# Performance work log

Hardware: AMD Instinct MI355X
Metric: run time of the kernel (lower is better)

Reference implementation:

```python
import jax, jax.numpy as jnp
import numpy as np

G = 128            # grid_size (hardcoded in NeRFRenderer.__init__)
T = 32             # time_size (reduced from 64 to keep working set < 4GB)
CAS = 1            # cascade = 1 + ceil(log2(bound)), bound = 1
DECAY = 0.95
DENSITY_SCALE = 1.0
DENSITY_THRESH = 0.01


def _expand_bits(v):
    # instant-ngp style 10-bit -> 30-bit expansion (works for 7-bit coords of G=128)
    v = (v * jnp.uint32(0x00010001)) & jnp.uint32(0xFF0000FF)
    v = (v * jnp.uint32(0x00000101)) & jnp.uint32(0x0F00F00F)
    v = (v * jnp.uint32(0x00000011)) & jnp.uint32(0xC30C30C3)
    v = (v * jnp.uint32(0x00000005)) & jnp.uint32(0x49249249)
    return v


def _morton3d(coords):
    # coords: [N, 3] int32 in [0, G)
    x = _expand_bits(coords[:, 0].astype(jnp.uint32))
    y = _expand_bits(coords[:, 1].astype(jnp.uint32))
    z = _expand_bits(coords[:, 2].astype(jnp.uint32))
    return (x | (y << 1) | (z << 2)).astype(jnp.int32)


def setup_inputs() -> dict:
    key = jax.random.key(0)
    k1, k2 = jax.random.split(key)
    density_grid = jax.random.normal(k1, (T, CAS, G ** 3), dtype=jnp.float32) * 0.5
    sigmas = jax.random.uniform(k2, (T, CAS, G ** 3), dtype=jnp.float32)
    return {"density_grid": density_grid, "sigmas": sigmas}


def reference(density_grid, sigmas):
    # full-grid branch of update_extra_state (iter_density < 16)
    g = jnp.arange(G, dtype=jnp.int32)
    xx, yy, zz = jnp.meshgrid(g, g, g, indexing='ij')
    coords = jnp.stack([xx.ravel(), yy.ravel(), zz.ravel()], axis=-1)  # [G^3, 3]
    indices = _morton3d(coords)                                        # [G^3]

    # tmp_grid = -1; tmp_grid[t, cas, indices] = sigmas * density_scale
    tmp_grid = -jnp.ones_like(density_grid)
    tmp_grid = tmp_grid.at[:, :, indices].set(sigmas * DENSITY_SCALE)

    # decay / max merge on mutually-valid cells
    valid = (density_grid >= 0) & (tmp_grid >= 0)
    new_grid = jnp.where(valid, jnp.maximum(density_grid * DECAY, tmp_grid), density_grid)

    # threshold + packbits into bitfield (8 cells per byte, morton order)
    mean_density = jnp.mean(jnp.clip(new_grid, 0.0))
    thresh = jnp.minimum(mean_density, jnp.float32(DENSITY_THRESH))
    bits = (new_grid > thresh).reshape(T, -1, 8)                       # [T, CAS*G^3/8, 8]
    weights = (jnp.int32(1) << jnp.arange(8, dtype=jnp.int32))
    bitfield = jnp.sum(bits.astype(jnp.int32) * weights, axis=-1)      # [T, CAS*G^3/8]
    return new_grid, bitfield
```

## Files before the change

### kernel.cpp

```cpp
#include <hip/hip_runtime.h>

#define G    128
#define G3   (G * G * G)
#define TDIM 32
#define NTOT (TDIM * G3)
#define NBYTES_OUT (NTOT / 8)
#define DECAY 0.95f
#define DTH   0.01f
#define NBLK1 (TDIM * 512)

__device__ __forceinline__ unsigned expand3(unsigned v) {
    v = (v * 0x00010001u) & 0xFF0000FFu;
    v = (v * 0x00000101u) & 0x0F00F00Fu;
    v = (v * 0x00000011u) & 0xC30C30C3u;
    v = (v * 0x00000005u) & 0x49249249u;
    return v;
}

__device__ __forceinline__ unsigned compact3(unsigned v) {
    v &= 0x49249249u;
    v = (v | (v >> 2))  & 0xC30C30C3u;
    v = (v | (v >> 4))  & 0x0F00F00Fu;
    v = (v | (v >> 8))  & 0xFF0000FFu;
    v = (v | (v >> 16)) & 0x000003FFu;
    return v;
}

__global__ __launch_bounds__(256) void
pass1(const float* __restrict__ dg, const float* __restrict__ sg,
      float* __restrict__ out_grid, float* __restrict__ out_bits,
      float* __restrict__ partials)
{
    __shared__ float smem[4096];
    const int blk  = blockIdx.x;
    const int t    = blk >> 9;
    const int cube = blk & 511;
    const int base = t * G3;

    const unsigned Xc = compact3((unsigned)cube);
    const unsigned Yc = compact3((unsigned)cube >> 1);
    const unsigned Zc = compact3((unsigned)cube >> 2);
    const int origin  = (int)((Xc << 18) | (Yc << 11) | (Zc << 4));
    const float* __restrict__ sgt = sg + base + origin;

    #pragma unroll
    for (int k = 0; k < 4; ++k) {
        const int c  = threadIdx.x + (k << 8);
        const int lx = c >> 6;
        const int ly = (c >> 2) & 15;
        const int lz = (c & 3) << 2;
        const float4 s = *reinterpret_cast<const float4*>(sgt + (lx << 14) + (ly << 7) + lz);
        const int m = (int)(expand3((unsigned)lx) | (expand3((unsigned)ly) << 1)
                          | (expand3((unsigned)lz) << 2));
        const int x = (((m >> 7) & 1) << 2) ^ (((m >> 8) & 1) << 3) ^ (((m >> 10) & 1) << 4);
        smem[m ^ x]        = s.x;
        smem[(m | 4) ^ x]  = s.y;
        smem[(m | 32) ^ x] = s.z;
        smem[(m | 36) ^ x] = s.w;
    }
    __syncthreads();

    float lsum = 0.f;
    #pragma unroll
    for (int k = 0; k < 4; ++k) {
        const int j  = (threadIdx.x + (k << 8)) << 2;
        const int xb = (((j >> 7) & 1) << 2) ^ (((j >> 8) & 1) << 3) ^ (((j >> 10) & 1) << 4);
        const float4 s = *reinterpret_cast<const float4*>(&smem[j ^ xb]);

        const int jg = base + (cube << 12) + j;
        const float4 v = *reinterpret_cast<const float4*>(dg + jg);

        float4 r;
        r.x = (v.x >= 0.f && s.x >= 0.f) ? fmaxf(v.x * DECAY, s.x) : v.x;
        r.y = (v.y >= 0.f && s.y >= 0.f) ? fmaxf(v.y * DECAY, s.y) : v.y;
        r.z = (v.z >= 0.f && s.z >= 0.f) ? fmaxf(v.z * DECAY, s.z) : v.z;
        r.w = (v.w >= 0.f && s.w >= 0.f) ? fmaxf(v.w * DECAY, s.w) : v.w;

        *reinterpret_cast<float4*>(out_grid + jg) = r;

        lsum += fmaxf(r.x, 0.f) + fmaxf(r.y, 0.f) + fmaxf(r.z, 0.f) + fmaxf(r.w, 0.f);

        int nib = (r.x > DTH ? 1 : 0) | (r.y > DTH ? 2 : 0) |
                  (r.z > DTH ? 4 : 0) | (r.w > DTH ? 8 : 0);
        int partner = __shfl_xor(nib, 1, 64);
        if ((threadIdx.x & 1) == 0)
            out_bits[jg >> 3] = (float)(nib | (partner << 4));
    }

    #pragma unroll
    for (int off = 32; off; off >>= 1) lsum += __shfl_down(lsum, off, 64);
    __shared__ float wsum[4];
    if ((threadIdx.x & 63) == 0) wsum[threadIdx.x >> 6] = lsum;
    __syncthreads();
    if (threadIdx.x == 0)
        partials[blk] = wsum[0] + wsum[1] + wsum[2] + wsum[3];
}

__global__ __launch_bounds__(1024) void
reduce_thresh(const float* __restrict__ partials, float* __restrict__ thresh)
{
    float s = 0.f;
    for (int i = threadIdx.x; i < NBLK1; i += 1024) s += partials[i];
    #pragma unroll
    for (int off = 32; off; off >>= 1) s += __shfl_down(s, off, 64);
    __shared__ float wsum[16];
    if ((threadIdx.x & 63) == 0) wsum[threadIdx.x >> 6] = s;
    __syncthreads();
    if (threadIdx.x == 0) {
        float tot = 0.f;
        #pragma unroll
        for (int i = 0; i < 16; ++i) tot += wsum[i];
        thresh[0] = fminf(tot / (float)NTOT, DTH);
    }
}

__global__ __launch_bounds__(256) void
fix_bits(const float* __restrict__ grid, const float* __restrict__ thresh,
         float* __restrict__ out_bits)
{
    const float th = thresh[0];
    if (th == DTH) return;
    const int n = blockIdx.x * 256 + threadIdx.x;
    const float4* g = reinterpret_cast<const float4*>(grid) + (n << 1);
    const float4 a = g[0], b = g[1];
    int byte = (a.x > th ? 1 : 0)   | (a.y > th ? 2 : 0)   |
               (a.z > th ? 4 : 0)   | (a.w > th ? 8 : 0)   |
               (b.x > th ? 16 : 0)  | (b.y > th ? 32 : 0)  |
               (b.z > th ? 64 : 0)  | (b.w > th ? 128 : 0);
    out_bits[n] = (float)byte;
}

extern "C" void kernel_launch(void* const* d_in, const int* in_sizes, int n_in,
                              void* d_out, int out_size, void* d_ws, size_t ws_size,
                              hipStream_t stream)
{
    const float* dg = (const float*)d_in[0];
    const float* sg = (const float*)d_in[1];
    float* out_grid = (float*)d_out;
    float* out_bits = out_grid + NTOT;
    float* partials = (float*)d_ws;
    float* thresh   = partials + NBLK1;

    pass1<<<NBLK1, 256, 0, stream>>>(dg, sg, out_grid, out_bits, partials);
    reduce_thresh<<<1, 1024, 0, stream>>>(partials, thresh);
    fix_bits<<<NBYTES_OUT / 256, 256, 0, stream>>>(out_grid, thresh, out_bits);
}
```

Before: 178.3 us.

## Issue density loads before the smem transpose, give each thread 16 contiguous cells, use nontemporal I/O

Each thread now owns 16 contiguous cells instead of four strided float4s. Its density_grid loads are issued at kernel start, before the sigma gather and barrier, so their latency overlaps the shared-memory transpose. Loads and stores use nontemporal builtins, and each thread writes two bitfield bytes directly, with no cross-lane shuffle. The launch bounds now request 6 waves per EU, and holding 16 values per thread raises register pressure. The per-thread contiguous access also changes the coalescing pattern of global memory traffic.

New measurement: 261.3 us. +46.5%, slower.

```diff
diff --git a/kernel.cpp b/kernel.cpp
--- a/kernel.cpp
+++ b/kernel.cpp
@@ -9,6 +9,9 @@
 #define DTH   0.01f
 #define NBLK1 (TDIM * 512)
 
+typedef float f32x4 __attribute__((ext_vector_type(4)));
+typedef float f32x2 __attribute__((ext_vector_type(2)));
+
 __device__ __forceinline__ unsigned expand3(unsigned v) {
     v = (v * 0x00010001u) & 0xFF0000FFu;
     v = (v * 0x00000101u) & 0x0F00F00Fu;
@@ -16,7 +19,6 @@
     v = (v * 0x00000005u) & 0x49249249u;
     return v;
 }
-
 __device__ __forceinline__ unsigned compact3(unsigned v) {
     v &= 0x49249249u;
     v = (v | (v >> 2))  & 0xC30C30C3u;
@@ -25,74 +27,99 @@
     v = (v | (v >> 16)) & 0x000003FFu;
     return v;
 }
+__device__ __forceinline__ int swz(int m) {
+    return (((m >> 7) & 1) << 2) ^ (((m >> 8) & 1) << 3) ^ (((m >> 10) & 1) << 4);
+}
 
-__global__ __launch_bounds__(256) void
+__device__ __forceinline__ f32x4 merge4(f32x4 v, f32x4 s) {
+    f32x4 r;
+    r.x = (v.x >= 0.f && s.x >= 0.f) ? fmaxf(v.x * DECAY, s.x) : v.x;
+    r.y = (v.y >= 0.f && s.y >= 0.f) ? fmaxf(v.y * DECAY, s.y) : v.y;
+    r.z = (v.z >= 0.f && s.z >= 0.f) ? fmaxf(v.z * DECAY, s.z) : v.z;
+    r.w = (v.w >= 0.f && s.w >= 0.f) ? fmaxf(v.w * DECAY, s.w) : v.w;
+    return r;
+}
+
+__global__ __launch_bounds__(256, 6) void
 pass1(const float* __restrict__ dg, const float* __restrict__ sg,
       float* __restrict__ out_grid, float* __restrict__ out_bits,
       float* __restrict__ partials)
 {
     __shared__ float smem[4096];
+    __shared__ float wsum[4];
     const int blk  = blockIdx.x;
     const int t    = blk >> 9;
     const int cube = blk & 511;
     const int base = t * G3;
+    const int tid  = threadIdx.x;
+    const int jg0  = base + (cube << 12) + (tid << 4);
+
+    const f32x4* dgp = reinterpret_cast<const f32x4*>(dg + jg0);
+    const f32x4 v0 = __builtin_nontemporal_load(dgp + 0);
+    const f32x4 v1 = __builtin_nontemporal_load(dgp + 1);
+    const f32x4 v2 = __builtin_nontemporal_load(dgp + 2);
+    const f32x4 v3 = __builtin_nontemporal_load(dgp + 3);
 
     const unsigned Xc = compact3((unsigned)cube);
     const unsigned Yc = compact3((unsigned)cube >> 1);
     const unsigned Zc = compact3((unsigned)cube >> 2);
-    const int origin  = (int)((Xc << 18) | (Yc << 11) | (Zc << 4));
-    const float* __restrict__ sgt = sg + base + origin;
-
+    const float* __restrict__ sgt = sg + base + (int)((Xc << 18) | (Yc << 11) | (Zc << 4));
     #pragma unroll
     for (int k = 0; k < 4; ++k) {
-        const int c  = threadIdx.x + (k << 8);
+        const int c  = tid + (k << 8);
         const int lx = c >> 6;
         const int ly = (c >> 2) & 15;
         const int lz = (c & 3) << 2;
-        const float4 s = *reinterpret_cast<const float4*>(sgt + (lx << 14) + (ly << 7) + lz);
-        const int m = (int)(expand3((unsigned)lx) | (expand3((unsigned)ly) << 1)
-                          | (expand3((unsigned)lz) << 2));
-        const int x = (((m >> 7) & 1) << 2) ^ (((m >> 8) & 1) << 3) ^ (((m >> 10) & 1) << 4);
-        smem[m ^ x]        = s.x;
-        smem[(m | 4) ^ x]  = s.y;
-        smem[(m | 32) ^ x] = s.z;
-        smem[(m | 36) ^ x] = s.w;
+        const f32x4 s = *reinterpret_cast<const f32x4*>(sgt + (lx << 14) + (ly << 7) + lz);
+        const int m  = (int)(expand3((unsigned)lx) | (expand3((unsigned)ly) << 1)
+                           | (expand3((unsigned)lz) << 2));
+        const int mb = m ^ swz(m);
+        smem[mb]      = s.x;
+        smem[mb ^ 4]  = s.y;
+        smem[mb ^ 32] = s.z;
+        smem[mb ^ 36] = s.w;
     }
     __syncthreads();
 
-    float lsum = 0.f;
-    #pragma unroll
-    for (int k = 0; k < 4; ++k) {
-        const int j  = (threadIdx.x + (k << 8)) << 2;
-        const int xb = (((j >> 7) & 1) << 2) ^ (((j >> 8) & 1) << 3) ^ (((j >> 10) & 1) << 4);
-        const float4 s = *reinterpret_cast<const float4*>(&smem[j ^ xb]);
+    const int j = tid << 4;
+    const int b = j ^ swz(j);
+    const f32x4 s0 = *reinterpret_cast<const f32x4*>(&smem[b]);
+    const f32x4 s1 = *reinterpret_cast<const f32x4*>(&smem[b ^ 4]);
+    const f32x4 s2 = *reinterpret_cast<const f32x4*>(&smem[b ^ 8]);
+    const f32x4 s3 = *reinterpret_cast<const f32x4*>(&smem[b ^ 12]);
 
-        const int jg = base + (cube << 12) + j;
-        const float4 v = *reinterpret_cast<const float4*>(dg + jg);
+    const f32x4 r0 = merge4(v0, s0);
+    const f32x4 r1 = merge4(v1, s1);
+    const f32x4 r2 = merge4(v2, s2);
+    const f32x4 r3 = merge4(v3, s3);
 
-        float4 r;
-        r.x = (v.x >= 0.f && s.x >= 0.f) ? fmaxf(v.x * DECAY, s.x) : v.x;
-        r.y = (v.y >= 0.f && s.y >= 0.f) ? fmaxf(v.y * DECAY, s.y) : v.y;
-        r.z = (v.z >= 0.f && s.z >= 0.f) ? fmaxf(v.z * DECAY, s.z) : v.z;
-        r.w = (v.w >= 0.f && s.w >= 0.f) ? fmaxf(v.w * DECAY, s.w) : v.w;
+    f32x4* ogp = reinterpret_cast<f32x4*>(out_grid + jg0);
+    __builtin_nontemporal_store(r0, ogp + 0);
+    __builtin_nontemporal_store(r1, ogp + 1);
+    __builtin_nontemporal_store(r2, ogp + 2);
+    __builtin_nontemporal_store(r3, ogp + 3);
 
-        *reinterpret_cast<float4*>(out_grid + jg) = r;
+    float lsum = fmaxf(r0.x, 0.f) + fmaxf(r0.y, 0.f) + fmaxf(r0.z, 0.f) + fmaxf(r0.w, 0.f)
+               + fmaxf(r1.x, 0.f) + fmaxf(r1.y, 0.f) + fmaxf(r1.z, 0.f) + fmaxf(r1.w, 0.f)
+               + fmaxf(r2.x, 0.f) + fmaxf(r2.y, 0.f) + fmaxf(r2.z, 0.f) + fmaxf(r2.w, 0.f)
+               + fmaxf(r3.x, 0.f) + fmaxf(r3.y, 0.f) + fmaxf(r3.z, 0.f) + fmaxf(r3.w, 0.f);
 
-        lsum += fmaxf(r.x, 0.f) + fmaxf(r.y, 0.f) + fmaxf(r.z, 0.f) + fmaxf(r.w, 0.f);
-
-        int nib = (r.x > DTH ? 1 : 0) | (r.y > DTH ? 2 : 0) |
-                  (r.z > DTH ? 4 : 0) | (r.w > DTH ? 8 : 0);
-        int partner = __shfl_xor(nib, 1, 64);
-        if ((threadIdx.x & 1) == 0)
-            out_bits[jg >> 3] = (float)(nib | (partner << 4));
-    }
+    const int byte0 = (r0.x > DTH ? 1 : 0)  | (r0.y > DTH ? 2 : 0)  |
+                      (r0.z > DTH ? 4 : 0)  | (r0.w > DTH ? 8 : 0)  |
+                      (r1.x > DTH ? 16 : 0) | (r1.y > DTH ? 32 : 0) |
+                      (r1.z > DTH ? 64 : 0) | (r1.w > DTH ? 128 : 0);
+    const int byte1 = (r2.x > DTH ? 1 : 0)  | (r2.y > DTH ? 2 : 0)  |
+                      (r2.z > DTH ? 4 : 0)  | (r2.w > DTH ? 8 : 0)  |
+                      (r3.x > DTH ? 16 : 0) | (r3.y > DTH ? 32 : 0) |
+                      (r3.z > DTH ? 64 : 0) | (r3.w > DTH ? 128 : 0);
+    f32x2 bb; bb.x = (float)byte0; bb.y = (float)byte1;
+    __builtin_nontemporal_store(bb, reinterpret_cast<f32x2*>(out_bits + (jg0 >> 3)));
 
     #pragma unroll
     for (int off = 32; off; off >>= 1) lsum += __shfl_down(lsum, off, 64);
-    __shared__ float wsum[4];
-    if ((threadIdx.x & 63) == 0) wsum[threadIdx.x >> 6] = lsum;
+    if ((tid & 63) == 0) wsum[tid >> 6] = lsum;
     __syncthreads();
-    if (threadIdx.x == 0)
+    if (tid == 0)
         partials[blk] = wsum[0] + wsum[1] + wsum[2] + wsum[3];
 }
 
```
